# Performance work log

Measured on AMD Instinct MI355X. Metric: run time of the kernel, lower is better.

## Reference

```python
import jax, jax.numpy as jnp
import numpy as np

N, D, T = 4096, 512, 4096
TEMPERATURE = 0.07
MARGIN = 0.5
CONT_WEIGHT = 1.0
TRIP_WEIGHT = 0.3
EPS = 1e-8        # eps in the log / denominator (matches torch code)
PD_EPS = 1e-6     # F.pairwise_distance default eps added to the difference


def setup_inputs() -> dict:
    key = jax.random.key(0)
    k1, k2, k3 = jax.random.split(key, 3)
    embeddings = jax.random.normal(k1, (N, D), dtype=jnp.float32)
    labels = jax.random.randint(k2, (N,), 0, 256)            # ~16 positives per place
    triplets = jax.random.randint(k3, (T, 3), 0, N)          # (anchor, pos, neg) indices
    return {"embeddings": embeddings, "labels": labels, "triplets": triplets}


def reference(embeddings, labels, triplets):
    # ---- MultiPositiveContrastiveLoss ----
    # F.cosine_similarity normalizes each row with eps=1e-8 on the norm.
    norms = jnp.linalg.norm(embeddings, axis=1, keepdims=True)
    n_emb = embeddings / jnp.maximum(norms, EPS)
    sim = (n_emb @ n_emb.T) / TEMPERATURE                    # [N, N]

    pos_mask = (labels[:, None] == labels[None, :]).astype(embeddings.dtype)
    pos_mask = pos_mask * (1.0 - jnp.eye(sim.shape[0], dtype=embeddings.dtype))

    exp_sim = jnp.exp(sim)
    pos_sum = (exp_sim * pos_mask).sum(axis=1)
    total_sum = exp_sim.sum(axis=1)
    loss = -jnp.log(pos_sum / (total_sum + EPS) + EPS)

    valid = pos_mask.sum(axis=1) > 0
    cnt = valid.sum()
    cont_loss = jnp.where(
        cnt > 0,
        jnp.where(valid, loss, 0.0).sum() / jnp.maximum(cnt, 1).astype(loss.dtype),
        jnp.zeros((), loss.dtype),
    )

    # ---- TripletLoss, vectorized over all triplets (replaces Python loop) ----
    a = embeddings[triplets[:, 0]]   # [T, D]
    p = embeddings[triplets[:, 1]]
    ng = embeddings[triplets[:, 2]]
    pos_dist = jnp.linalg.norm(a - p + PD_EPS, axis=1)
    neg_dist = jnp.linalg.norm(a - ng + PD_EPS, axis=1)
    trip_loss = jnp.maximum(pos_dist - neg_dist + MARGIN, 0.0).mean()

    total = CONT_WEIGHT * cont_loss + TRIP_WEIGHT * trip_loss
    return (total, cont_loss, trip_loss)
```

## Files before the change

kernel.cpp:

```cpp
#include <hip/hip_runtime.h>

#define NN 4096
#define DD 512
#define TT 4096

typedef __bf16 bf16x8 __attribute__((ext_vector_type(8)));
typedef float f32x4 __attribute__((ext_vector_type(4)));

constexpr float INV_TEMP = 1.0f / 0.07f;

#define AS1(p) ((__attribute__((address_space(1))) const void*)(p))
#define AS3(p) ((__attribute__((address_space(3))) void*)(p))

__global__ __launch_bounds__(256) void k_normtrip(const float* __restrict__ emb,
                                                  __bf16* __restrict__ nemb,
                                                  const int* __restrict__ trip,
                                                  float* __restrict__ tl) {
    int wave = threadIdx.x >> 6, lane = threadIdx.x & 63;
    int row = blockIdx.x * 4 + wave;

    int ia = trip[row * 3 + 0], ip = trip[row * 3 + 1], ig = trip[row * 3 + 2];
    const float4* pa = (const float4*)(emb + (size_t)ia * DD);
    const float4* pp = (const float4*)(emb + (size_t)ip * DD);
    const float4* pn = (const float4*)(emb + (size_t)ig * DD);
    float d1 = 0.0f, d2 = 0.0f;
    #pragma unroll
    for (int j = 0; j < 2; ++j) {
        float4 a = pa[lane * 2 + j];
        float4 p = pp[lane * 2 + j];
        float4 n = pn[lane * 2 + j];
        float dx;
        dx = a.x - p.x + 1e-6f; d1 += dx * dx;
        dx = a.y - p.y + 1e-6f; d1 += dx * dx;
        dx = a.z - p.z + 1e-6f; d1 += dx * dx;
        dx = a.w - p.w + 1e-6f; d1 += dx * dx;
        dx = a.x - n.x + 1e-6f; d2 += dx * dx;
        dx = a.y - n.y + 1e-6f; d2 += dx * dx;
        dx = a.z - n.z + 1e-6f; d2 += dx * dx;
        dx = a.w - n.w + 1e-6f; d2 += dx * dx;
    }

    const float4* src = (const float4*)(emb + (size_t)row * DD);
    float4 x0 = src[lane * 2 + 0];
    float4 x1 = src[lane * 2 + 1];
    float ss = x0.x * x0.x + x0.y * x0.y + x0.z * x0.z + x0.w * x0.w +
               x1.x * x1.x + x1.y * x1.y + x1.z * x1.z + x1.w * x1.w;
    #pragma unroll
    for (int m = 1; m < 64; m <<= 1) ss += __shfl_xor(ss, m, 64);
    float inv = 1.0f / fmaxf(sqrtf(ss), 1e-8f);
    bf16x8 v;
    v[0] = (__bf16)(x0.x * inv); v[1] = (__bf16)(x0.y * inv);
    v[2] = (__bf16)(x0.z * inv); v[3] = (__bf16)(x0.w * inv);
    v[4] = (__bf16)(x1.x * inv); v[5] = (__bf16)(x1.y * inv);
    v[6] = (__bf16)(x1.z * inv); v[7] = (__bf16)(x1.w * inv);
    *(bf16x8*)(nemb + (size_t)row * DD + lane * 8) = v;

    #pragma unroll
    for (int m = 1; m < 64; m <<= 1) {
        d1 += __shfl_xor(d1, m, 64);
        d2 += __shfl_xor(d2, m, 64);
    }
    if (lane == 0) tl[row] = fmaxf(sqrtf(d1) - sqrtf(d2) + 0.5f, 0.0f);
}


__global__ __launch_bounds__(256, 2) void k_contrast(const __bf16* __restrict__ nemb,
                                                     const int* __restrict__ labels,
                                                     float* __restrict__ posP,
                                                     float* __restrict__ totP) {
    __shared__ __attribute__((aligned(16))) __bf16 aS[2][128 * 64];
    __shared__ __attribute__((aligned(16))) __bf16 bS[2][128 * 64];
    __shared__ int rlab[128];
    __shared__ int clab[128];

    int tid = threadIdx.x;
    int lane = tid & 63, wave = tid >> 6;
    int wr = wave >> 1, wc = wave & 1;
    int l15 = lane & 15, quad = lane >> 4;
    int swz = l15 & 7;

    int t = (blockIdx.x & 7) * 66 + (blockIdx.x >> 3);
    int r = 0;
    while (t >= 32 - r) { t -= 32 - r; ++r; }
    int c = r + t;
    int row0 = r * 128, col0 = c * 128;

    if (tid < 128) rlab[tid] = labels[row0 + tid];
    else if (tid < 256) clab[tid - 128] = labels[col0 + tid - 128];

    int srr = (tid >> 3) & 7;
    int scol = ((tid & 7) ^ srr) * 8;
    const __bf16* gA0 = nemb + (size_t)(row0 + wave * 32 + srr) * DD + scol;
    const __bf16* gB0 = nemb + (size_t)(col0 + wave * 32 + srr) * DD + scol;
    int ldst = wave * 2048 + (tid & 63) * 8;

    f32x4 acc[4][4];
    #pragma unroll
    for (int fm = 0; fm < 4; ++fm)
        #pragma unroll
        for (int fn = 0; fn < 4; ++fn) {
            f32x4 z = {0.0f, 0.0f, 0.0f, 0.0f};
            acc[fm][fn] = z;
        }

    #pragma unroll
    for (int j = 0; j < 4; ++j) {
        __builtin_amdgcn_global_load_lds(AS1(gA0 + (size_t)(j * 8) * DD),
                                         AS3(&aS[0][ldst + j * 512]), 16, 0, 0);
        __builtin_amdgcn_global_load_lds(AS1(gB0 + (size_t)(j * 8) * DD),
                                         AS3(&bS[0][ldst + j * 512]), 16, 0, 0);
    }
    __syncthreads();

    #pragma unroll
    for (int kt = 0; kt < 8; ++kt) {
        int cur = kt & 1;
        if (kt < 7) {
            #pragma unroll
            for (int j = 0; j < 4; ++j) {
                __builtin_amdgcn_global_load_lds(AS1(gA0 + (size_t)(j * 8) * DD + (kt + 1) * 64),
                                                 AS3(&aS[cur ^ 1][ldst + j * 512]), 16, 0, 0);
                __builtin_amdgcn_global_load_lds(AS1(gB0 + (size_t)(j * 8) * DD + (kt + 1) * 64),
                                                 AS3(&bS[cur ^ 1][ldst + j * 512]), 16, 0, 0);
            }
        }
        #pragma unroll
        for (int kc = 0; kc < 2; ++kc) {
            bf16x8 af[4], bf[4];
            #pragma unroll
            for (int fm = 0; fm < 4; ++fm)
                af[fm] = *(const bf16x8*)(&aS[cur][(wr * 64 + fm * 16 + l15) * 64 +
                                                   (((kc * 4 + quad) ^ swz) * 8)]);
            #pragma unroll
            for (int fn = 0; fn < 4; ++fn)
                bf[fn] = *(const bf16x8*)(&bS[cur][(wc * 64 + fn * 16 + l15) * 64 +
                                                   (((kc * 4 + quad) ^ swz) * 8)]);
            #pragma unroll
            for (int fm = 0; fm < 4; ++fm)
                #pragma unroll
                for (int fn = 0; fn < 4; ++fn)
                    acc[fm][fn] = __builtin_amdgcn_mfma_f32_16x16x32_bf16(
                        af[fm], bf[fn], acc[fm][fn], 0, 0, 0);
        }
        __syncthreads();
    }

    float tc[4] = {0, 0, 0, 0}, pc[4] = {0, 0, 0, 0};
    #pragma unroll
    for (int fm = 0; fm < 4; ++fm) {
        int rloc = wr * 64 + fm * 16 + quad * 4;
        int gibase = row0 + rloc;
        int rl[4];
        #pragma unroll
        for (int v = 0; v < 4; ++v) rl[v] = rlab[rloc + v];
        float tv[4] = {0, 0, 0, 0}, pv[4] = {0, 0, 0, 0};
        #pragma unroll
        for (int fn = 0; fn < 4; ++fn) {
            int cloc = wc * 64 + fn * 16 + l15;
            int cl = clab[cloc];
            int gj = col0 + cloc;
            f32x4 a = acc[fm][fn];
            #pragma unroll
            for (int v = 0; v < 4; ++v) {
                float e = __expf(a[v] * INV_TEMP);
                tv[v] += e;
                bool match = (rl[v] == cl) && ((gibase + v) != gj);
                float pe = match ? e : 0.0f;
                pv[v] += pe;
                tc[fn] += e;
                pc[fn] += pe;
            }
        }
        #pragma unroll
        for (int m = 1; m < 16; m <<= 1) {
            #pragma unroll
            for (int v = 0; v < 4; ++v) {
                tv[v] += __shfl_xor(tv[v], m, 64);
                pv[v] += __shfl_xor(pv[v], m, 64);
            }
        }
        if (l15 == 0) {
            #pragma unroll
            for (int v = 0; v < 4; ++v) {
                int o = (gibase + v) * 64 + c * 2 + wc;
                posP[o] = pv[v];
                totP[o] = tv[v];
            }
        }
    }

    if (r != c) {
        #pragma unroll
        for (int fn = 0; fn < 4; ++fn) {
            tc[fn] += __shfl_xor(tc[fn], 16, 64);
            tc[fn] += __shfl_xor(tc[fn], 32, 64);
            pc[fn] += __shfl_xor(pc[fn], 16, 64);
            pc[fn] += __shfl_xor(pc[fn], 32, 64);
        }
        if (quad == 0) {
            #pragma unroll
            for (int fn = 0; fn < 4; ++fn) {
                int gcol = col0 + wc * 64 + fn * 16 + l15;
                int o = gcol * 64 + r * 2 + wr;
                posP[o] = pc[fn];
                totP[o] = tc[fn];
            }
        }
    }
}

__global__ __launch_bounds__(256) void k_rowloss(const float* __restrict__ posP,
                                                 const float* __restrict__ totP,
                                                 const int* __restrict__ labels,
                                                 float* __restrict__ rloss,
                                                 float* __restrict__ rvalid) {
    __shared__ int hist[256];
    int tid = threadIdx.x;
    hist[tid] = 0;
    __syncthreads();
    #pragma unroll
    for (int j = 0; j < 16; ++j)
        atomicAdd(&hist[labels[tid + j * 256]], 1);
    __syncthreads();

    int wave = tid >> 6, lane = tid & 63;
    int row = blockIdx.x * 4 + wave;
    float p = posP[row * 64 + lane];
    float t = totP[row * 64 + lane];
    #pragma unroll
    for (int m = 1; m < 64; m <<= 1) {
        p += __shfl_xor(p, m, 64);
        t += __shfl_xor(t, m, 64);
    }
    if (lane == 0) {
        bool valid = hist[labels[row]] > 1;
        float loss = valid ? -logf(p / (t + 1e-8f) + 1e-8f) : 0.0f;
        rloss[row] = loss;
        rvalid[row] = valid ? 1.0f : 0.0f;
    }
}

__global__ __launch_bounds__(256) void k_final(const float* __restrict__ rloss,
                                               const float* __restrict__ rvalid,
                                               const float* __restrict__ tl,
                                               float* __restrict__ out) {
    int tid = threadIdx.x;
    float sl = 0.0f, sv = 0.0f, st = 0.0f;
    for (int i = tid; i < NN; i += 256) {
        sl += rloss[i];
        sv += rvalid[i];
        st += tl[i];
    }
    #pragma unroll
    for (int m = 1; m < 64; m <<= 1) {
        sl += __shfl_xor(sl, m, 64);
        sv += __shfl_xor(sv, m, 64);
        st += __shfl_xor(st, m, 64);
    }
    __shared__ float red[3][4];
    int lane = tid & 63, wave = tid >> 6;
    if (lane == 0) { red[0][wave] = sl; red[1][wave] = sv; red[2][wave] = st; }
    __syncthreads();
    if (tid == 0) {
        float SL = red[0][0] + red[0][1] + red[0][2] + red[0][3];
        float SV = red[1][0] + red[1][1] + red[1][2] + red[1][3];
        float ST = red[2][0] + red[2][1] + red[2][2] + red[2][3];
        float cont = (SV > 0.0f) ? (SL / SV) : 0.0f;
        float trip = ST * (1.0f / (float)TT);
        out[0] = cont + 0.3f * trip;
        out[1] = cont;
        out[2] = trip;
    }
}

extern "C" void kernel_launch(void* const* d_in, const int* in_sizes, int n_in,
                              void* d_out, int out_size, void* d_ws, size_t ws_size,
                              hipStream_t stream) {
    const float* emb = (const float*)d_in[0];
    const int* labels = (const int*)d_in[1];
    const int* trips = (const int*)d_in[2];
    float* out = (float*)d_out;
    char* ws = (char*)d_ws;

    __bf16* nemb  = (__bf16*)(ws);
    float* posP   = (float*)(ws + 4194304);
    float* totP   = (float*)(ws + 5242880);
    float* rloss  = (float*)(ws + 6291456);
    float* rvalid = (float*)(ws + 6307840);
    float* tl     = (float*)(ws + 6324224);

    k_normtrip<<<NN / 4, 256, 0, stream>>>(emb, nemb, trips, tl);
    k_contrast<<<528, 256, 0, stream>>>(nemb, labels, posP, totP);
    k_rowloss<<<NN / 4, 256, 0, stream>>>(posP, totP, labels, rloss, rvalid);
    k_final<<<1, 256, 0, stream>>>(rloss, rvalid, tl, out);
}
```

Before: 101.2 us.

## Split contrast tiles into 128x64 halves with 2-wave blocks, single-buffered LDS

```diff
diff --git a/kernel.cpp b/kernel.cpp
--- a/kernel.cpp
+++ b/kernel.cpp
@@ -64,35 +64,36 @@
 }
 
 
-__global__ __launch_bounds__(256, 2) void k_contrast(const __bf16* __restrict__ nemb,
+__global__ __launch_bounds__(128, 3) void k_contrast(const __bf16* __restrict__ nemb,
                                                      const int* __restrict__ labels,
                                                      float* __restrict__ posP,
                                                      float* __restrict__ totP) {
-    __shared__ __attribute__((aligned(16))) __bf16 aS[2][128 * 64];
-    __shared__ __attribute__((aligned(16))) __bf16 bS[2][128 * 64];
+    __shared__ __attribute__((aligned(16))) __bf16 aS[128 * 64];
+    __shared__ __attribute__((aligned(16))) __bf16 bS[64 * 64];
     __shared__ int rlab[128];
-    __shared__ int clab[128];
+    __shared__ int clab[64];
 
     int tid = threadIdx.x;
     int lane = tid & 63, wave = tid >> 6;
-    int wr = wave >> 1, wc = wave & 1;
     int l15 = lane & 15, quad = lane >> 4;
     int swz = l15 & 7;
 
-    int t = (blockIdx.x & 7) * 66 + (blockIdx.x >> 3);
+    int u = (blockIdx.x & 7) * 132 + (blockIdx.x >> 3);
+    int t = u >> 1, ch = u & 1;
     int r = 0;
     while (t >= 32 - r) { t -= 32 - r; ++r; }
     int c = r + t;
     int row0 = r * 128, col0 = c * 128;
-
-    if (tid < 128) rlab[tid] = labels[row0 + tid];
-    else if (tid < 256) clab[tid - 128] = labels[col0 + tid - 128];
+    int cb0 = col0 + ch * 64;
+
+    rlab[tid] = labels[row0 + tid];
+    if (tid < 64) clab[tid] = labels[cb0 + tid];
 
     int srr = (tid >> 3) & 7;
     int scol = ((tid & 7) ^ srr) * 8;
-    const __bf16* gA0 = nemb + (size_t)(row0 + wave * 32 + srr) * DD + scol;
-    const __bf16* gB0 = nemb + (size_t)(col0 + wave * 32 + srr) * DD + scol;
-    int ldst = wave * 2048 + (tid & 63) * 8;
+    const __bf16* gA0 = nemb + (size_t)(row0 + (tid >> 3)) * DD + scol;
+    const __bf16* gB0 = nemb + (size_t)(cb0 + (tid >> 3)) * DD + scol;
+    int ldst = tid * 8;
 
     f32x4 acc[4][4];
     #pragma unroll
@@ -104,37 +105,27 @@
         }
 
     #pragma unroll
-    for (int j = 0; j < 4; ++j) {
-        __builtin_amdgcn_global_load_lds(AS1(gA0 + (size_t)(j * 8) * DD),
-                                         AS3(&aS[0][ldst + j * 512]), 16, 0, 0);
-        __builtin_amdgcn_global_load_lds(AS1(gB0 + (size_t)(j * 8) * DD),
-                                         AS3(&bS[0][ldst + j * 512]), 16, 0, 0);
-    }
-    __syncthreads();
-
-    #pragma unroll
     for (int kt = 0; kt < 8; ++kt) {
-        int cur = kt & 1;
-        if (kt < 7) {
-            #pragma unroll
-            for (int j = 0; j < 4; ++j) {
-                __builtin_amdgcn_global_load_lds(AS1(gA0 + (size_t)(j * 8) * DD + (kt + 1) * 64),
-                                                 AS3(&aS[cur ^ 1][ldst + j * 512]), 16, 0, 0);
-                __builtin_amdgcn_global_load_lds(AS1(gB0 + (size_t)(j * 8) * DD + (kt + 1) * 64),
-                                                 AS3(&bS[cur ^ 1][ldst + j * 512]), 16, 0, 0);
-            }
-        }
+        #pragma unroll
+        for (int j = 0; j < 8; ++j)
+            __builtin_amdgcn_global_load_lds(AS1(gA0 + (size_t)(j * 16) * DD + kt * 64),
+                                             AS3(&aS[ldst + j * 1024]), 16, 0, 0);
+        #pragma unroll
+        for (int j = 0; j < 4; ++j)
+            __builtin_amdgcn_global_load_lds(AS1(gB0 + (size_t)(j * 16) * DD + kt * 64),
+                                             AS3(&bS[ldst + j * 1024]), 16, 0, 0);
+        __syncthreads();
         #pragma unroll
         for (int kc = 0; kc < 2; ++kc) {
             bf16x8 af[4], bf[4];
             #pragma unroll
             for (int fm = 0; fm < 4; ++fm)
-                af[fm] = *(const bf16x8*)(&aS[cur][(wr * 64 + fm * 16 + l15) * 64 +
-                                                   (((kc * 4 + quad) ^ swz) * 8)]);
+                af[fm] = *(const bf16x8*)(&aS[(wave * 64 + fm * 16 + l15) * 64 +
+                                              (((kc * 4 + quad) ^ swz) * 8)]);
             #pragma unroll
             for (int fn = 0; fn < 4; ++fn)
-                bf[fn] = *(const bf16x8*)(&bS[cur][(wc * 64 + fn * 16 + l15) * 64 +
-                                                   (((kc * 4 + quad) ^ swz) * 8)]);
+                bf[fn] = *(const bf16x8*)(&bS[(fn * 16 + l15) * 64 +
+                                              (((kc * 4 + quad) ^ swz) * 8)]);
             #pragma unroll
             for (int fm = 0; fm < 4; ++fm)
                 #pragma unroll
@@ -142,13 +133,13 @@
                     acc[fm][fn] = __builtin_amdgcn_mfma_f32_16x16x32_bf16(
                         af[fm], bf[fn], acc[fm][fn], 0, 0, 0);
         }
-        __syncthreads();
+        if (kt < 7) __syncthreads();
     }
 
     float tc[4] = {0, 0, 0, 0}, pc[4] = {0, 0, 0, 0};
     #pragma unroll
     for (int fm = 0; fm < 4; ++fm) {
-        int rloc = wr * 64 + fm * 16 + quad * 4;
+        int rloc = wave * 64 + fm * 16 + quad * 4;
         int gibase = row0 + rloc;
         int rl[4];
         #pragma unroll
@@ -156,9 +147,9 @@
         float tv[4] = {0, 0, 0, 0}, pv[4] = {0, 0, 0, 0};
         #pragma unroll
         for (int fn = 0; fn < 4; ++fn) {
-            int cloc = wc * 64 + fn * 16 + l15;
+            int cloc = fn * 16 + l15;
             int cl = clab[cloc];
-            int gj = col0 + cloc;
+            int gj = cb0 + cloc;
             f32x4 a = acc[fm][fn];
             #pragma unroll
             for (int v = 0; v < 4; ++v) {
@@ -182,7 +173,7 @@
         if (l15 == 0) {
             #pragma unroll
             for (int v = 0; v < 4; ++v) {
-                int o = (gibase + v) * 64 + c * 2 + wc;
+                int o = (gibase + v) * 64 + c * 2 + ch;
                 posP[o] = pv[v];
                 totP[o] = tv[v];
             }
@@ -200,8 +191,8 @@
         if (quad == 0) {
             #pragma unroll
             for (int fn = 0; fn < 4; ++fn) {
-                int gcol = col0 + wc * 64 + fn * 16 + l15;
-                int o = gcol * 64 + r * 2 + wr;
+                int gcol = cb0 + fn * 16 + l15;
+                int o = gcol * 64 + r * 2 + wave;
                 posP[o] = pc[fn];
                 totP[o] = tc[fn];
             }
@@ -290,7 +281,7 @@
     float* tl     = (float*)(ws + 6324224);
 
     k_normtrip<<<NN / 4, 256, 0, stream>>>(emb, nemb, trips, tl);
-    k_contrast<<<528, 256, 0, stream>>>(nemb, labels, posP, totP);
+    k_contrast<<<1056, 128, 0, stream>>>(nemb, labels, posP, totP);
     k_rowloss<<<NN / 4, 256, 0, stream>>>(posP, totP, labels, rloss, rvalid);
     k_final<<<1, 256, 0, stream>>>(rloss, rvalid, tl, out);
 }
```

New measurement: 95.49 us (median of 3 runs). 5.6% less time.
